# Kernel tuning notes

Hardware: AMD Instinct MI355X
Metric: run time of the kernel (lower is better)

## Reference

```python
import jax, jax.numpy as jnp
import numpy as np

DIM = 1536
NUM_HEADS = 16
HEAD_DIM = DIM // NUM_HEADS  # 96
ROPE_DIM = HEAD_DIM // 2     # 48
PT_SEQ = 32
FT_SEQ = 32
EPS = 1e-6


def _rope_tables():
    # VisionRotaryEmbedding(dim=48, pt_seq_len=32): 2D axial rotary tables
    f = 1.0 / (10000.0 ** (np.arange(0, ROPE_DIM, 2, dtype=np.float32)[: ROPE_DIM // 2] / ROPE_DIM))
    pos = np.arange(FT_SEQ, dtype=np.float32) / FT_SEQ * PT_SEQ
    freqs = pos[:, None] * f[None, :]                       # [32, 24]
    freqs = np.repeat(freqs, 2, axis=-1)                    # [32, 48] interleaved
    row = np.broadcast_to(freqs[:, None, :], (FT_SEQ, FT_SEQ, ROPE_DIM))
    col = np.broadcast_to(freqs[None, :, :], (FT_SEQ, FT_SEQ, ROPE_DIM))
    grid = np.concatenate([row, col], axis=-1).reshape(-1, HEAD_DIM)  # [1024, 96]
    return jnp.asarray(np.cos(grid)), jnp.asarray(np.sin(grid))


def _apply_rotary(x, cos, sin):
    # x: [B, S, H, D]; cos/sin: [S, D]; interleaved (use_real_unbind_dim=-1) rotation
    xr = x.reshape(*x.shape[:-1], -1, 2)
    x_rot = jnp.stack([-xr[..., 1], xr[..., 0]], axis=-1).reshape(x.shape)
    return x * cos[None, :, None, :] + x_rot * sin[None, :, None, :]


def _rms_norm(x, w):
    var = jnp.mean(jnp.square(x), axis=-1, keepdims=True)
    return x * jax.lax.rsqrt(var + EPS) * w


def setup_inputs() -> dict:
    key = jax.random.key(0)
    ks = jax.random.split(key, 12)
    s = 1.0 / np.sqrt(DIM)
    return {
        "hidden_states": jax.random.normal(ks[0], (8, 1024, DIM), dtype=jnp.float32),
        "Wq": jax.random.normal(ks[1], (DIM, DIM), dtype=jnp.float32) * s,
        "bq": jax.random.normal(ks[2], (DIM,), dtype=jnp.float32) * 0.01,
        "Wk": jax.random.normal(ks[3], (DIM, DIM), dtype=jnp.float32) * s,
        "bk": jax.random.normal(ks[4], (DIM,), dtype=jnp.float32) * 0.01,
        "Wv": jax.random.normal(ks[5], (DIM, DIM), dtype=jnp.float32) * s,
        "bv": jax.random.normal(ks[6], (DIM,), dtype=jnp.float32) * 0.01,
        "q_norm_w": jnp.ones((HEAD_DIM,), dtype=jnp.float32),
        "k_norm_w": jnp.ones((HEAD_DIM,), dtype=jnp.float32),
        "Wo": jax.random.normal(ks[7], (DIM, DIM), dtype=jnp.float32) * s,
        "bo": jax.random.normal(ks[8], (DIM,), dtype=jnp.float32) * 0.01,
    }


def reference(hidden_states, Wq, bq, Wk, bk, Wv, bv, q_norm_w, k_norm_w, Wo, bo):
    B, S, _ = hidden_states.shape
    cos, sin = _rope_tables()  # [S, HEAD_DIM], constants

    q = hidden_states @ Wq.T + bq
    k = hidden_states @ Wk.T + bk
    v = hidden_states @ Wv.T + bv
    q = q.reshape(B, S, NUM_HEADS, HEAD_DIM)
    k = k.reshape(B, S, NUM_HEADS, HEAD_DIM)
    v = v.reshape(B, S, NUM_HEADS, HEAD_DIM)

    q = _rms_norm(q, q_norm_w)
    k = _rms_norm(k, k_norm_w)
    q = _apply_rotary(q, cos, sin)
    k = _apply_rotary(k, cos, sin)

    scale = 1.0 / np.sqrt(HEAD_DIM)
    scores = jnp.einsum("bshd,bthd->bhst", q, k) * scale  # [B, H, S, S]
    probs = jax.nn.softmax(scores, axis=-1)
    out = jnp.einsum("bhst,bthd->bshd", probs, v)          # [B, S, H, D]
    out = out.reshape(B, S, DIM)
    return out @ Wo.T + bo
```

## Files before the change

### kernel.cpp

```cpp
#include <hip/hip_runtime.h>
#include <hip/hip_bf16.h>
#include <math.h>

typedef __hip_bfloat16 bf16;
typedef __attribute__((ext_vector_type(8))) short short8;
typedef __attribute__((ext_vector_type(4))) float f32x4;

#define MFMA16(a, b, c) __builtin_amdgcn_mfma_f32_16x16x32_bf16((a), (b), (c), 0, 0, 0)

typedef const __attribute__((address_space(1))) void GVOID;
typedef __attribute__((address_space(3))) void LVOID;

__device__ __forceinline__ float b2f(short s) {
    union { unsigned u; float f; } v;
    v.u = ((unsigned)(unsigned short)s) << 16;
    return v.f;
}
__device__ __forceinline__ short f2b(float f) {
    union { float f; unsigned u; } v;
    v.f = f;
    unsigned r = v.u + 0x7fffu + ((v.u >> 16) & 1u);
    return (short)(r >> 16);
}

__global__ void sniff_kernel(const unsigned* __restrict__ X, int* __restrict__ flag) {
    __shared__ int cnt;
    if (threadIdx.x == 0) cnt = 0;
    __syncthreads();
    int c = 0;
    for (int i = threadIdx.x; i < 256; i += 64) {
        unsigned w = X[i];
        unsigned e = (w >> 7) & 0xFFu;
        c += (e > 140u) ? 1 : 0;
    }
    atomicAdd(&cnt, c);
    __syncthreads();
    if (threadIdx.x == 0) *flag = (cnt >= 16) ? 1 : 0;
}

__device__ __forceinline__ void canon8(const void* src, short* dst, int i, int f) {
    short8 o;
    if (f) {
        const float* s = (const float*)src + (size_t)i * 8;
#pragma unroll
        for (int j = 0; j < 8; ++j) o[j] = f2b(s[j]);
    } else {
        o = ((const short8*)src)[i];
    }
    ((short8*)dst)[i] = o;
}

__global__ __launch_bounds__(256) void canon_x_kernel(
    const void* __restrict__ src, short* __restrict__ dst, int n8,
    const int* __restrict__ flag)
{
    int i = blockIdx.x * 256 + threadIdx.x;
    if (i >= n8) return;
    canon8(src, dst, i, *flag);
}

__global__ __launch_bounds__(256) void canon_w4_kernel(
    const void* __restrict__ s0, const void* __restrict__ s1,
    const void* __restrict__ s2, const void* __restrict__ s3,
    short* __restrict__ d0, short* __restrict__ d1,
    short* __restrict__ d2, short* __restrict__ d3,
    const int* __restrict__ flag)
{
    const int m = blockIdx.y;
    const void* src = (m == 0) ? s0 : (m == 1) ? s1 : (m == 2) ? s2 : s3;
    short* dst = (m == 0) ? d0 : (m == 1) ? d1 : (m == 2) ? d2 : d3;
    int i = blockIdx.x * 256 + threadIdx.x;
    canon8(src, dst, i, *flag);
}

__global__ void canon_vec_kernel(
    const void* __restrict__ bq, const void* __restrict__ bk,
    const void* __restrict__ bv, const void* __restrict__ bo,
    const void* __restrict__ qw, const void* __restrict__ kw,
    float* __restrict__ biasqkv, float* __restrict__ boc,
    float* __restrict__ qwc, float* __restrict__ kwc,
    const int* __restrict__ flag)
{
    const int f = *flag;
    for (int i = threadIdx.x; i < 6336; i += 256) {
        const void* src; float* dst; int j;
        if (i < 4608) {
            int m = i / 1536; j = i - m * 1536;
            src = (m == 0) ? bq : (m == 1) ? bk : bv; dst = biasqkv + i;
        } else if (i < 6144) { j = i - 4608; src = bo; dst = boc + j; }
        else if (i < 6240)   { j = i - 6144; src = qw; dst = qwc + j; }
        else                 { j = i - 6240; src = kw; dst = kwc + j; }
        *dst = f ? ((const float*)src)[j] : b2f(((const short*)src)[j]);
    }
}

__global__ void rope_tables_kernel(float* __restrict__ cosT, float* __restrict__ sinT) {
    int idx = blockIdx.x * 256 + threadIdx.x;
    if (idx >= 1024 * 96) return;
    int p = idx / 96;
    int d = idx - p * 96;
    int r = p >> 5, c = p & 31;
    int inRow = (d < 48);
    int dd = inRow ? d : d - 48;
    float pos = inRow ? (float)r : (float)c;
    float ex = -(float)(dd & ~1) / 48.0f;
    float f = powf(10000.0f, ex);
    float ang = pos * f;
    cosT[idx] = cosf(ang);
    sinT[idx] = sinf(ang);
}

__global__ __launch_bounds__(512) void gemm256_kernel(
    const bf16* __restrict__ A, const bf16* __restrict__ Bw,
    const float* __restrict__ bias,
    bf16* __restrict__ O0, bf16* __restrict__ O1, bf16* __restrict__ O2,
    int K, const int* __restrict__ outFlag)
{
    __shared__ __align__(16) short As[2][256 * 64];
    __shared__ __align__(16) short Bs[2][256 * 64];

    const int tid = threadIdx.x;
    const int lane = tid & 63, w = tid >> 6;
    const int wm = w >> 2, wn = w & 3;
    const int li = lane & 15, lg = lane >> 4;

    const int total = gridDim.x * gridDim.y;
    const int pp = blockIdx.y * gridDim.x + blockIdx.x;
    const int lb = (pp & 7) * (total >> 3) + (pp >> 3);
    const int nb = lb % gridDim.x;
    const int mb = lb / gridDim.x;
    const long mBase = (long)mb * 256;
    const long nGlob = (long)nb * 256;

    const bf16* aSrc[4]; const bf16* bSrc[4]; int ldsOff[4];
#pragma unroll
    for (int u = 0; u < 4; ++u) {
        const int L = u * 8192 + tid * 16;
        const int S = L ^ (((L >> 7) & 7) << 4);
        const int srow = S >> 7;
        const int scol = (S & 127) >> 1;
        aSrc[u] = A + (mBase + srow) * K + scol;
        bSrc[u] = Bw + (nGlob + srow) * K + scol;
        ldsOff[u] = L >> 1;
    }

    const int rxor = (li & 7) << 4;
    int kidx[2];
#pragma unroll
    for (int ks = 0; ks < 2; ++ks)
        kidx[ks] = ((ks * 64 + lg * 16) ^ rxor) >> 1;

    f32x4 acc[8][4] = {};
    const int NT = K >> 6;

    auto stage = [&](int tt, int bb) {
        const long kc = (long)tt * 64;
#pragma unroll
        for (int u = 0; u < 4; ++u)
            __builtin_amdgcn_global_load_lds((GVOID*)(aSrc[u] + kc),
                                             (LVOID*)&As[bb][ldsOff[u]], 16, 0, 0);
#pragma unroll
        for (int u = 0; u < 4; ++u)
            __builtin_amdgcn_global_load_lds((GVOID*)(bSrc[u] + kc),
                                             (LVOID*)&Bs[bb][ldsOff[u]], 16, 0, 0);
    };

    stage(0, 0);
    asm volatile("s_waitcnt vmcnt(0)" ::: "memory");
    __builtin_amdgcn_s_barrier();
    asm volatile("" ::: "memory");

    for (int t = 0; t < NT; ++t) {
        const int cb = t & 1;
        if (t + 1 < NT) stage(t + 1, cb ^ 1);
        const short* Ab = &As[cb][0];
        const short* Bb = &Bs[cb][0];
        short8 fa[4][2], fb[2][2];
#pragma unroll
        for (int ph = 0; ph < 4; ++ph) {
            const int qm = ph >> 1, qn = ph & 1;
            if (qn == 0) {
#pragma unroll
                for (int m = 0; m < 4; ++m) {
                    const int row = wm * 128 + (qm * 4 + m) * 16 + li;
#pragma unroll
                    for (int ks = 0; ks < 2; ++ks)
                        fa[m][ks] = *(const short8*)(Ab + row * 64 + kidx[ks]);
                }
            }
#pragma unroll
            for (int n = 0; n < 2; ++n) {
                const int row = wn * 64 + (qn * 2 + n) * 16 + li;
#pragma unroll
                for (int ks = 0; ks < 2; ++ks)
                    fb[n][ks] = *(const short8*)(Bb + row * 64 + kidx[ks]);
            }
            __builtin_amdgcn_sched_barrier(0);
            __builtin_amdgcn_s_setprio(1);
#pragma unroll
            for (int m = 0; m < 4; ++m)
#pragma unroll
                for (int n = 0; n < 2; ++n)
#pragma unroll
                    for (int ks = 0; ks < 2; ++ks)
                        acc[qm * 4 + m][qn * 2 + n] =
                            MFMA16(fa[m][ks], fb[n][ks], acc[qm * 4 + m][qn * 2 + n]);
            __builtin_amdgcn_s_setprio(0);
            __builtin_amdgcn_sched_barrier(0);
        }
        asm volatile("s_waitcnt vmcnt(0)" ::: "memory");
        __builtin_amdgcn_s_barrier();
        asm volatile("" ::: "memory");
    }

    const int f32out = outFlag ? *outFlag : 0;
    const int mat = nb / 6;
    const long colBase = nGlob - (long)mat * 1536;
    bf16* Ob = (mat == 0) ? O0 : (mat == 1) ? O1 : O2;
    if (f32out) {
        float* Cf = (float*)Ob;
#pragma unroll
        for (int n = 0; n < 4; ++n) {
            const long col = colBase + wn * 64 + n * 16 + li;
            const float bv = bias[nGlob + wn * 64 + n * 16 + li];
#pragma unroll
            for (int m = 0; m < 8; ++m) {
                const long row = mBase + wm * 128 + m * 16 + lg * 4;
#pragma unroll
                for (int i = 0; i < 4; ++i)
                    Cf[(row + i) * 1536 + col] = acc[m][n][i] + bv;
            }
        }
    } else {
#pragma unroll
        for (int n = 0; n < 4; ++n) {
            const long col = colBase + wn * 64 + n * 16 + li;
            const float bv = bias[nGlob + wn * 64 + n * 16 + li];
#pragma unroll
            for (int m = 0; m < 8; ++m) {
                const long row = mBase + wm * 128 + m * 16 + lg * 4;
#pragma unroll
                for (int i = 0; i < 4; ++i)
                    Ob[(row + i) * 1536 + col] = __float2bfloat16(acc[m][n][i] + bv);
            }
        }
    }
}

__global__ __launch_bounds__(256) void norm_rope_kernel(
    bf16* __restrict__ T, const float* __restrict__ wgt,
    const float* __restrict__ cosT, const float* __restrict__ sinT,
    float scale)
{
    const int row = blockIdx.x * 256 + threadIdx.x;
    const int tok = row >> 4;
    const int h = row & 15;
    const int spos = tok & 1023;
    bf16* p = T + (size_t)tok * 1536 + h * 96;

    float x[96];
#pragma unroll
    for (int v = 0; v < 12; ++v) {
        short8 t = *(const short8*)(p + v * 8);
#pragma unroll
        for (int j = 0; j < 8; ++j) x[v * 8 + j] = b2f(t[j]);
    }
    float ss = 0.f;
#pragma unroll
    for (int d = 0; d < 96; ++d) ss += x[d] * x[d];
    const float rn = scale / sqrtf(ss * (1.0f / 96.0f) + 1e-6f);

    const float* cr = cosT + spos * 96;
    const float* sr = sinT + spos * 96;

#pragma unroll
    for (int v = 0; v < 12; ++v) {
        short8 o;
#pragma unroll
        for (int j = 0; j < 8; j += 2) {
            const int d = v * 8 + j;
            const float x0 = x[d] * rn * wgt[d];
            const float x1 = x[d + 1] * rn * wgt[d + 1];
            o[j]     = f2b(x0 * cr[d] - x1 * sr[d]);
            o[j + 1] = f2b(x1 * cr[d + 1] + x0 * sr[d + 1]);
        }
        *(short8*)(p + v * 8) = o;
    }
}

__global__ __launch_bounds__(256) void attn_kernel(
    const bf16* __restrict__ Q, const bf16* __restrict__ K,
    const bf16* __restrict__ V, bf16* __restrict__ O)
{
    __shared__ __align__(16) short Ks[64 * 100];
    __shared__ __align__(16) short Vt[96 * 76];
    __shared__ __align__(16) short Pl[4][32 * 72];

    const int tid = threadIdx.x;
    const int l = tid & 63, w = tid >> 6;
    const int li = l & 15, lg = l >> 4;

    const int p = blockIdx.x;
    const int lb = (p & 7) * 128 + (p >> 3);
    const int qt = lb & 7;
    const int bh = lb >> 3;
    const int b = bh >> 4, h = bh & 15;
    const size_t tokBase = (size_t)b * 1024;

    short8 aq[2][3];
#pragma unroll
    for (int r = 0; r < 2; ++r) {
        const bf16* qp = Q + (tokBase + qt * 128 + w * 32 + r * 16 + li) * 1536 + h * 96;
#pragma unroll
        for (int kk = 0; kk < 3; ++kk)
            aq[r][kk] = *(const short8*)(qp + kk * 32 + lg * 8);
    }

    float m_r[2][4], l_r[2][4];
#pragma unroll
    for (int r = 0; r < 2; ++r)
#pragma unroll
        for (int i = 0; i < 4; ++i) { m_r[r][i] = -1e30f; l_r[r][i] = 0.f; }
    f32x4 o[2][6] = {};

    int kr[3], km[3];
#pragma unroll
    for (int u = 0; u < 3; ++u) {
        const int c = tid + 256 * u;
        kr[u] = c / 12;
        km[u] = (c - kr[u] * 12) * 8;
    }
    const int vr = tid >> 2;
    const int vc0 = (tid & 3) * 24;
    short* Plw = &Pl[w][0];

    for (int t0 = 0; t0 < 1024; t0 += 64) {
        __syncthreads();
#pragma unroll
        for (int u = 0; u < 3; ++u) {
            short8 t = *(const short8*)(K + (tokBase + t0 + kr[u]) * 1536 + h * 96 + km[u]);
            *(short8*)&Ks[kr[u] * 100 + km[u]] = t;
        }
        const bf16* vp = V + (tokBase + t0 + vr) * 1536 + h * 96 + vc0;
#pragma unroll
        for (int u = 0; u < 3; ++u) {
            short8 t = *(const short8*)(vp + u * 8);
#pragma unroll
            for (int j = 0; j < 8; ++j)
                Vt[(vc0 + u * 8 + j) * 76 + vr] = t[j];
        }
        __syncthreads();

        f32x4 s4[2][4] = {};
#pragma unroll
        for (int kk = 0; kk < 3; ++kk) {
            short8 fb[4];
#pragma unroll
            for (int kn = 0; kn < 4; ++kn)
                fb[kn] = *(const short8*)&Ks[(kn * 16 + li) * 100 + kk * 32 + lg * 8];
#pragma unroll
            for (int r = 0; r < 2; ++r)
#pragma unroll
                for (int kn = 0; kn < 4; ++kn)
                    s4[r][kn] = MFMA16(aq[r][kk], fb[kn], s4[r][kn]);
        }

#pragma unroll
        for (int r = 0; r < 2; ++r) {
            float alpha[4];
            bool need = false;
#pragma unroll
            for (int i = 0; i < 4; ++i) {
                float pm = fmaxf(fmaxf(s4[r][0][i], s4[r][1][i]),
                                 fmaxf(s4[r][2][i], s4[r][3][i]));
#pragma unroll
                for (int msk = 1; msk < 16; msk <<= 1)
                    pm = fmaxf(pm, __shfl_xor(pm, msk));
                const float mo = m_r[r][i];
                if (pm > mo + 8.0f) {
                    alpha[i] = exp2f(mo - pm);
                    m_r[r][i] = pm;
                    need = true;
                } else {
                    alpha[i] = 1.0f;
                }
                const float mn = m_r[r][i];
                float rs = 0.f;
#pragma unroll
                for (int kn = 0; kn < 4; ++kn) {
                    const float pv = exp2f(s4[r][kn][i] - mn);
                    rs += pv;
                    Plw[(r * 16 + lg * 4 + i) * 72 + kn * 16 + li] = f2b(pv);
                }
#pragma unroll
                for (int msk = 1; msk < 16; msk <<= 1)
                    rs += __shfl_xor(rs, msk);
                l_r[r][i] = l_r[r][i] * alpha[i] + rs;
            }
            if (need) {
#pragma unroll
                for (int dn = 0; dn < 6; ++dn)
#pragma unroll
                    for (int i = 0; i < 4; ++i) o[r][dn][i] *= alpha[i];
            }
        }

#pragma unroll
        for (int kt = 0; kt < 2; ++kt) {
            short8 pa[2];
#pragma unroll
            for (int r = 0; r < 2; ++r)
                pa[r] = *(const short8*)&Plw[(r * 16 + li) * 72 + kt * 32 + lg * 8];
#pragma unroll
            for (int dn = 0; dn < 6; ++dn) {
                short8 fv = *(const short8*)&Vt[(dn * 16 + li) * 76 + kt * 32 + lg * 8];
#pragma unroll
                for (int r = 0; r < 2; ++r)
                    o[r][dn] = MFMA16(pa[r], fv, o[r][dn]);
            }
        }
    }

#pragma unroll
    for (int r = 0; r < 2; ++r)
#pragma unroll
        for (int dn = 0; dn < 6; ++dn)
#pragma unroll
            for (int i = 0; i < 4; ++i) {
                const size_t row = tokBase + qt * 128 + w * 32 + r * 16 + lg * 4 + i;
                O[row * 1536 + h * 96 + dn * 16 + li] =
                    __float2bfloat16(o[r][dn][i] / l_r[r][i]);
            }
}

extern "C" void kernel_launch(void* const* d_in, const int* in_sizes, int n_in,
                              void* d_out, int out_size, void* d_ws, size_t ws_size,
                              hipStream_t stream) {
    const void* X  = d_in[0];
    const void* Wq = d_in[1];
    const void* bq = d_in[2];
    const void* Wk = d_in[3];
    const void* bk = d_in[4];
    const void* Wv = d_in[5];
    const void* bv = d_in[6];
    const void* qw = d_in[7];
    const void* kw = d_in[8];
    const void* Wo = d_in[9];
    const void* bo = d_in[10];

    char* ws = (char*)d_ws;
    size_t off = 0;
    int* flag = (int*)ws;                      off += 256;
    float* cosT = (float*)(ws + off);          off += 1024 * 96 * 4;
    float* sinT = (float*)(ws + off);          off += 1024 * 96 * 4;
    float* biasqkv = (float*)(ws + off);       off += 4608 * 4;
    float* boc  = (float*)(ws + off);          off += 1536 * 4;
    float* qwc  = (float*)(ws + off);          off += 128 * 4;
    float* kwc  = (float*)(ws + off);          off += 128 * 4;
    off = (off + 255) & ~(size_t)255;
    bf16* Wc  = (bf16*)(ws + off);             off += (size_t)4608 * 1536 * 2;
    bf16* Woc = (bf16*)(ws + off);             off += (size_t)1536 * 1536 * 2;
    bf16* Xc  = (bf16*)(ws + off);             off += (size_t)8192 * 1536 * 2;
    bf16* Qb  = (bf16*)(ws + off);             off += (size_t)8192 * 1536 * 2;
    bf16* Kb  = (bf16*)(ws + off);             off += (size_t)8192 * 1536 * 2;
    bf16* Vb  = (bf16*)(ws + off);             off += (size_t)8192 * 1536 * 2;
    bf16* AO  = Xc;

    sniff_kernel<<<1, 64, 0, stream>>>((const unsigned*)X, flag);

    canon_x_kernel<<<6144, 256, 0, stream>>>(X, (short*)Xc, 8192 * 1536 / 8, flag);
    canon_w4_kernel<<<dim3(1152, 4), 256, 0, stream>>>(
        Wq, Wk, Wv, Wo,
        (short*)Wc, (short*)(Wc + (size_t)1536 * 1536), (short*)(Wc + (size_t)2 * 1536 * 1536),
        (short*)Woc, flag);
    canon_vec_kernel<<<1, 256, 0, stream>>>(bq, bk, bv, bo, qw, kw,
                                            biasqkv, boc, qwc, kwc, flag);
    rope_tables_kernel<<<384, 256, 0, stream>>>(cosT, sinT);

    gemm256_kernel<<<dim3(18, 32), 512, 0, stream>>>(
        Xc, Wc, biasqkv, Qb, Kb, Vb, 1536, nullptr);

    const float qscale = (float)(0.10206207261596577 * 1.4426950408889634);
    norm_rope_kernel<<<512, 256, 0, stream>>>(Qb, qwc, cosT, sinT, qscale);
    norm_rope_kernel<<<512, 256, 0, stream>>>(Kb, kwc, cosT, sinT, 1.0f);

    attn_kernel<<<1024, 256, 0, stream>>>(Qb, Kb, Vb, AO);

    gemm256_kernel<<<dim3(6, 32), 512, 0, stream>>>(
        AO, Woc, boc, (bf16*)d_out, (bf16*)d_out, (bf16*)d_out, 1536, flag);
}
```

Before: 434.7 us.

## Shrink GEMM K-tile, transpose attention MFMA layout, prefetch K/V into registers

```diff
diff --git a/kernel.cpp b/kernel.cpp
--- a/kernel.cpp
+++ b/kernel.cpp
@@ -4,6 +4,7 @@
 
 typedef __hip_bfloat16 bf16;
 typedef __attribute__((ext_vector_type(8))) short short8;
+typedef __attribute__((ext_vector_type(4))) short short4v;
 typedef __attribute__((ext_vector_type(4))) float f32x4;
 
 #define MFMA16(a, b, c) __builtin_amdgcn_mfma_f32_16x16x32_bf16((a), (b), (c), 0, 0, 0)
@@ -21,6 +22,9 @@
     v.f = f;
     unsigned r = v.u + 0x7fffu + ((v.u >> 16) & 1u);
     return (short)(r >> 16);
+}
+__device__ __forceinline__ unsigned packbf(float a, float b) {
+    return ((unsigned)(unsigned short)f2b(a)) | (((unsigned)(unsigned short)f2b(b)) << 16);
 }
 
 __global__ void sniff_kernel(const unsigned* __restrict__ X, int* __restrict__ flag) {
@@ -116,8 +120,8 @@
     bf16* __restrict__ O0, bf16* __restrict__ O1, bf16* __restrict__ O2,
     int K, const int* __restrict__ outFlag)
 {
-    __shared__ __align__(16) short As[2][256 * 64];
-    __shared__ __align__(16) short Bs[2][256 * 64];
+    __shared__ __align__(16) short As[2][256 * 32];
+    __shared__ __align__(16) short Bs[2][256 * 32];
 
     const int tid = threadIdx.x;
     const int lane = tid & 63, w = tid >> 6;
@@ -132,35 +136,30 @@
     const long mBase = (long)mb * 256;
     const long nGlob = (long)nb * 256;
 
-    const bf16* aSrc[4]; const bf16* bSrc[4]; int ldsOff[4];
-#pragma unroll
-    for (int u = 0; u < 4; ++u) {
+    const bf16* aSrc[2]; const bf16* bSrc[2]; int ldsOff[2];
+#pragma unroll
+    for (int u = 0; u < 2; ++u) {
         const int L = u * 8192 + tid * 16;
-        const int S = L ^ (((L >> 7) & 7) << 4);
-        const int srow = S >> 7;
-        const int scol = (S & 127) >> 1;
+        const int S = L ^ (((L >> 7) & 3) << 4);
+        const int srow = S >> 6;
+        const int scol = (S & 63) >> 1;
         aSrc[u] = A + (mBase + srow) * K + scol;
         bSrc[u] = Bw + (nGlob + srow) * K + scol;
         ldsOff[u] = L >> 1;
     }
-
-    const int rxor = (li & 7) << 4;
-    int kidx[2];
-#pragma unroll
-    for (int ks = 0; ks < 2; ++ks)
-        kidx[ks] = ((ks * 64 + lg * 16) ^ rxor) >> 1;
+    const int koff = ((lg * 16) ^ (((li >> 1) & 3) << 4)) >> 1;
 
     f32x4 acc[8][4] = {};
-    const int NT = K >> 6;
+    const int NT = K >> 5;
 
     auto stage = [&](int tt, int bb) {
-        const long kc = (long)tt * 64;
-#pragma unroll
-        for (int u = 0; u < 4; ++u)
+        const long kc = (long)tt * 32;
+#pragma unroll
+        for (int u = 0; u < 2; ++u)
             __builtin_amdgcn_global_load_lds((GVOID*)(aSrc[u] + kc),
                                              (LVOID*)&As[bb][ldsOff[u]], 16, 0, 0);
 #pragma unroll
-        for (int u = 0; u < 4; ++u)
+        for (int u = 0; u < 2; ++u)
             __builtin_amdgcn_global_load_lds((GVOID*)(bSrc[u] + kc),
                                              (LVOID*)&Bs[bb][ldsOff[u]], 16, 0, 0);
     };
@@ -175,39 +174,34 @@
         if (t + 1 < NT) stage(t + 1, cb ^ 1);
         const short* Ab = &As[cb][0];
         const short* Bb = &Bs[cb][0];
-        short8 fa[4][2], fb[2][2];
-#pragma unroll
-        for (int ph = 0; ph < 4; ++ph) {
-            const int qm = ph >> 1, qn = ph & 1;
-            if (qn == 0) {
-#pragma unroll
-                for (int m = 0; m < 4; ++m) {
-                    const int row = wm * 128 + (qm * 4 + m) * 16 + li;
-#pragma unroll
-                    for (int ks = 0; ks < 2; ++ks)
-                        fa[m][ks] = *(const short8*)(Ab + row * 64 + kidx[ks]);
-                }
-            }
-#pragma unroll
-            for (int n = 0; n < 2; ++n) {
-                const int row = wn * 64 + (qn * 2 + n) * 16 + li;
-#pragma unroll
-                for (int ks = 0; ks < 2; ++ks)
-                    fb[n][ks] = *(const short8*)(Bb + row * 64 + kidx[ks]);
-            }
-            __builtin_amdgcn_sched_barrier(0);
-            __builtin_amdgcn_s_setprio(1);
-#pragma unroll
-            for (int m = 0; m < 4; ++m)
-#pragma unroll
-                for (int n = 0; n < 2; ++n)
-#pragma unroll
-                    for (int ks = 0; ks < 2; ++ks)
-                        acc[qm * 4 + m][qn * 2 + n] =
-                            MFMA16(fa[m][ks], fb[n][ks], acc[qm * 4 + m][qn * 2 + n]);
-            __builtin_amdgcn_s_setprio(0);
-            __builtin_amdgcn_sched_barrier(0);
-        }
+        short8 fb[4], fa[4];
+#pragma unroll
+        for (int n = 0; n < 4; ++n)
+            fb[n] = *(const short8*)(Bb + (wn * 64 + n * 16 + li) * 32 + koff);
+#pragma unroll
+        for (int m = 0; m < 4; ++m)
+            fa[m] = *(const short8*)(Ab + (wm * 128 + m * 16 + li) * 32 + koff);
+        __builtin_amdgcn_sched_barrier(0);
+        __builtin_amdgcn_s_setprio(1);
+#pragma unroll
+        for (int m = 0; m < 4; ++m)
+#pragma unroll
+            for (int n = 0; n < 4; ++n)
+                acc[m][n] = MFMA16(fa[m], fb[n], acc[m][n]);
+        __builtin_amdgcn_s_setprio(0);
+        __builtin_amdgcn_sched_barrier(0);
+#pragma unroll
+        for (int m = 0; m < 4; ++m)
+            fa[m] = *(const short8*)(Ab + (wm * 128 + 64 + m * 16 + li) * 32 + koff);
+        __builtin_amdgcn_sched_barrier(0);
+        __builtin_amdgcn_s_setprio(1);
+#pragma unroll
+        for (int m = 0; m < 4; ++m)
+#pragma unroll
+            for (int n = 0; n < 4; ++n)
+                acc[4 + m][n] = MFMA16(fa[m], fb[n], acc[4 + m][n]);
+        __builtin_amdgcn_s_setprio(0);
+        __builtin_amdgcn_sched_barrier(0);
         asm volatile("s_waitcnt vmcnt(0)" ::: "memory");
         __builtin_amdgcn_s_barrier();
         asm volatile("" ::: "memory");
@@ -316,11 +310,8 @@
             aq[r][kk] = *(const short8*)(qp + kk * 32 + lg * 8);
     }
 
-    float m_r[2][4], l_r[2][4];
-#pragma unroll
-    for (int r = 0; r < 2; ++r)
-#pragma unroll
-        for (int i = 0; i < 4; ++i) { m_r[r][i] = -1e30f; l_r[r][i] = 0.f; }
+    float m_r[2] = {-1e30f, -1e30f};
+    float l_r[2] = {0.f, 0.f};
     f32x4 o[2][6] = {};
 
     int kr[3], km[3];
@@ -334,74 +325,96 @@
     const int vc0 = (tid & 3) * 24;
     short* Plw = &Pl[w][0];
 
+    short8 kreg[3], vreg[3];
+#pragma unroll
+    for (int u = 0; u < 3; ++u)
+        kreg[u] = *(const short8*)(K + (tokBase + kr[u]) * 1536 + h * 96 + km[u]);
+    {
+        const bf16* vp = V + (tokBase + vr) * 1536 + h * 96 + vc0;
+#pragma unroll
+        for (int u = 0; u < 3; ++u) vreg[u] = *(const short8*)(vp + u * 8);
+    }
+
     for (int t0 = 0; t0 < 1024; t0 += 64) {
         __syncthreads();
 #pragma unroll
-        for (int u = 0; u < 3; ++u) {
-            short8 t = *(const short8*)(K + (tokBase + t0 + kr[u]) * 1536 + h * 96 + km[u]);
-            *(short8*)&Ks[kr[u] * 100 + km[u]] = t;
-        }
-        const bf16* vp = V + (tokBase + t0 + vr) * 1536 + h * 96 + vc0;
-#pragma unroll
-        for (int u = 0; u < 3; ++u) {
-            short8 t = *(const short8*)(vp + u * 8);
+        for (int u = 0; u < 3; ++u)
+            *(short8*)&Ks[kr[u] * 100 + km[u]] = kreg[u];
+#pragma unroll
+        for (int u = 0; u < 3; ++u)
 #pragma unroll
             for (int j = 0; j < 8; ++j)
-                Vt[(vc0 + u * 8 + j) * 76 + vr] = t[j];
-        }
+                Vt[(vc0 + u * 8 + j) * 76 + vr] = vreg[u][j];
         __syncthreads();
 
+        const int t1 = (t0 + 64 < 1024) ? t0 + 64 : t0;
+#pragma unroll
+        for (int u = 0; u < 3; ++u)
+            kreg[u] = *(const short8*)(K + (tokBase + t1 + kr[u]) * 1536 + h * 96 + km[u]);
+        {
+            const bf16* vp = V + (tokBase + t1 + vr) * 1536 + h * 96 + vc0;
+#pragma unroll
+            for (int u = 0; u < 3; ++u) vreg[u] = *(const short8*)(vp + u * 8);
+        }
+
         f32x4 s4[2][4] = {};
 #pragma unroll
         for (int kk = 0; kk < 3; ++kk) {
-            short8 fb[4];
+            short8 fk[4];
 #pragma unroll
             for (int kn = 0; kn < 4; ++kn)
-                fb[kn] = *(const short8*)&Ks[(kn * 16 + li) * 100 + kk * 32 + lg * 8];
+                fk[kn] = *(const short8*)&Ks[(kn * 16 + li) * 100 + kk * 32 + lg * 8];
 #pragma unroll
             for (int r = 0; r < 2; ++r)
 #pragma unroll
                 for (int kn = 0; kn < 4; ++kn)
-                    s4[r][kn] = MFMA16(aq[r][kk], fb[kn], s4[r][kn]);
+                    s4[r][kn] = MFMA16(fk[kn], aq[r][kk], s4[r][kn]);
         }
 
 #pragma unroll
         for (int r = 0; r < 2; ++r) {
-            float alpha[4];
-            bool need = false;
-#pragma unroll
-            for (int i = 0; i < 4; ++i) {
-                float pm = fmaxf(fmaxf(s4[r][0][i], s4[r][1][i]),
-                                 fmaxf(s4[r][2][i], s4[r][3][i]));
-#pragma unroll
-                for (int msk = 1; msk < 16; msk <<= 1)
-                    pm = fmaxf(pm, __shfl_xor(pm, msk));
-                const float mo = m_r[r][i];
-                if (pm > mo + 8.0f) {
-                    alpha[i] = exp2f(mo - pm);
-                    m_r[r][i] = pm;
-                    need = true;
-                } else {
-                    alpha[i] = 1.0f;
-                }
-                const float mn = m_r[r][i];
-                float rs = 0.f;
-#pragma unroll
-                for (int kn = 0; kn < 4; ++kn) {
-                    const float pv = exp2f(s4[r][kn][i] - mn);
-                    rs += pv;
-                    Plw[(r * 16 + lg * 4 + i) * 72 + kn * 16 + li] = f2b(pv);
-                }
-#pragma unroll
-                for (int msk = 1; msk < 16; msk <<= 1)
-                    rs += __shfl_xor(rs, msk);
-                l_r[r][i] = l_r[r][i] * alpha[i] + rs;
+            float mk[4];
+#pragma unroll
+            for (int kn = 0; kn < 4; ++kn)
+                mk[kn] = fmaxf(fmaxf(s4[r][kn][0], s4[r][kn][1]),
+                               fmaxf(s4[r][kn][2], s4[r][kn][3]));
+            float pm = fmaxf(fmaxf(mk[0], mk[1]), fmaxf(mk[2], mk[3]));
+            pm = fmaxf(pm, __shfl_xor(pm, 16));
+            pm = fmaxf(pm, __shfl_xor(pm, 32));
+
+            float alpha = 1.0f;
+            const bool need = (pm > m_r[r] + 8.0f);
+            if (need) { alpha = exp2f(m_r[r] - pm); m_r[r] = pm; }
+            const float mn = m_r[r];
+
+            float rs = 0.f;
+            unsigned pw[8];
+#pragma unroll
+            for (int kn = 0; kn < 4; ++kn) {
+                float p0 = exp2f(s4[r][kn][0] - mn);
+                float p1 = exp2f(s4[r][kn][1] - mn);
+                float p2 = exp2f(s4[r][kn][2] - mn);
+                float p3 = exp2f(s4[r][kn][3] - mn);
+                rs += (p0 + p1) + (p2 + p3);
+                pw[kn * 2]     = packbf(p0, p1);
+                pw[kn * 2 + 1] = packbf(p2, p3);
             }
+            rs += __shfl_xor(rs, 16);
+            rs += __shfl_xor(rs, 32);
+            l_r[r] = l_r[r] * alpha + rs;
             if (need) {
 #pragma unroll
                 for (int dn = 0; dn < 6; ++dn)
 #pragma unroll
-                    for (int i = 0; i < 4; ++i) o[r][dn][i] *= alpha[i];
+                    for (int i = 0; i < 4; ++i) o[r][dn][i] *= alpha;
+            }
+            unsigned* Pw = (unsigned*)Plw;
+            const int rowW = ((r * 16 + li) * 72) >> 1;
+#pragma unroll
+            for (int kn = 0; kn < 4; ++kn) {
+#pragma unroll
+                for (int ip = 0; ip < 2; ++ip)
+                    Pw[rowW + ((kn * 16 + lg * 4 + ip * 2) >> 1)] = pw[kn * 2 + ip];
             }
         }
 
@@ -416,21 +429,23 @@
                 short8 fv = *(const short8*)&Vt[(dn * 16 + li) * 76 + kt * 32 + lg * 8];
 #pragma unroll
                 for (int r = 0; r < 2; ++r)
-                    o[r][dn] = MFMA16(pa[r], fv, o[r][dn]);
+                    o[r][dn] = MFMA16(fv, pa[r], o[r][dn]);
             }
         }
     }
 
 #pragma unroll
-    for (int r = 0; r < 2; ++r)
-#pragma unroll
-        for (int dn = 0; dn < 6; ++dn)
-#pragma unroll
-            for (int i = 0; i < 4; ++i) {
-                const size_t row = tokBase + qt * 128 + w * 32 + r * 16 + lg * 4 + i;
-                O[row * 1536 + h * 96 + dn * 16 + li] =
-                    __float2bfloat16(o[r][dn][i] / l_r[r][i]);
-            }
+    for (int r = 0; r < 2; ++r) {
+        const float inv = 1.0f / l_r[r];
+        const size_t row = tokBase + qt * 128 + w * 32 + r * 16 + li;
+#pragma unroll
+        for (int dn = 0; dn < 6; ++dn) {
+            short4v ov;
+#pragma unroll
+            for (int i = 0; i < 4; ++i) ov[i] = f2b(o[r][dn][i] * inv);
+            *(short4v*)&O[row * 1536 + h * 96 + dn * 16 + lg * 4] = ov;
+        }
+    }
 }
 
 extern "C" void kernel_launch(void* const* d_in, const int* in_sizes, int n_in,
```

Result: slower. 461.5 us (+6.2%).
